# Kernel tuning notes

Hardware: AMD Instinct MI355X
Metric: run time of the kernel (lower is better)

The kernel has to match this reference:

```python
import jax, jax.numpy as jnp
import numpy as np

N, E, H, D, FE = 50000, 400000, 4, 64, 64  # nodes, edges, heads, per-head dim, edge feat dim
NEG_SLOPE = 0.2


def setup_inputs() -> dict:
    key = jax.random.key(0)
    ks = jax.random.split(key, 18)
    def p(k, shape, s=0.1):
        return jax.random.normal(k, shape, dtype=jnp.float32) * s
    return dict(
        features=p(ks[0], (N, D), 1.0),
        edge_feat=p(ks[1], (E, FE), 1.0),
        src=jax.random.randint(ks[2], (E,), 0, N),
        dst=jax.random.randint(ks[3], (E,), 0, N),
        # layer 0: in=64 -> H*D=256, residual Linear since 64 != 256
        W0=p(ks[4], (D, H * D)), We0=p(ks[5], (FE, H * D)),
        al0=p(ks[6], (H, D)), ar0=p(ks[7], (H, D)), ae0=p(ks[8], (H, D)),
        b0=p(ks[9], (H * D,)), Wres0=p(ks[10], (D, H * D)),
        # layer 1 (last): in=256 -> H*D=256, residual = identity view
        W1=p(ks[11], (H * D, H * D)), We1=p(ks[12], (FE, H * D)),
        al1=p(ks[13], (H, D)), ar1=p(ks[14], (H, D)), ae1=p(ks[15], (H, D)),
        b1=p(ks[16], (H * D,)),
    )


def _edge_gat_layer(h, ef, src, dst, W, We, al, ar, ae, b, Wres=None):
    n = h.shape[0]
    ft = (h @ W).reshape(n, H, D)          # (N,H,D) projected node feats
    fe = (ef @ We).reshape(-1, H, D)       # (E,H,D) projected edge feats
    el = jnp.sum(ft * al, axis=-1)         # (N,H)
    er = jnp.sum(ft * ar, axis=-1)         # (N,H)
    ee = jnp.sum(fe * ae, axis=-1)         # (E,H)
    e = el[src] + er[dst] + ee             # (E,H)
    e = jnp.where(e > 0, e, NEG_SLOPE * e)  # leaky_relu(0.2)
    # segment softmax over incoming edges of each dst node
    m = jax.ops.segment_max(jax.lax.stop_gradient(e), dst, num_segments=n)
    ex = jnp.exp(e - m[dst])
    den = jax.ops.segment_sum(ex, dst, num_segments=n)
    a = ex / den[dst]                      # (E,H) attention
    out = jax.ops.segment_sum(ft[src] * a[:, :, None], dst, num_segments=n)  # (N,H,D)
    res = (h @ Wres).reshape(n, H, D) if Wres is not None else h.reshape(n, H, D)
    return out + res + b.reshape(1, H, D)


def reference(features, edge_feat, src, dst,
              W0, We0, al0, ar0, ae0, b0, Wres0,
              W1, We1, al1, ar1, ae1, b1):
    h = _edge_gat_layer(features, edge_feat, src, dst, W0, We0, al0, ar0, ae0, b0, Wres0)
    h = jax.nn.elu(h.reshape(N, H * D))    # flatten heads + ELU between layers
    h = _edge_gat_layer(h, edge_feat, src, dst, W1, We1, al1, ar1, ae1, b1)
    return h.mean(axis=1)                  # (N, D) mean over heads on last layer
```

## Files before the change

kernel.cpp:

```cpp
#include <hip/hip_runtime.h>
#include <hip/hip_bf16.h>

#define NN 50000
#define EE 400000
#define NB 196

typedef __bf16 bf16_8 __attribute__((ext_vector_type(8)));
typedef __bf16 bf16_4 __attribute__((ext_vector_type(4)));
typedef __bf16 bf16_2 __attribute__((ext_vector_type(2)));
typedef float f32x4 __attribute__((ext_vector_type(4)));
typedef float f32x2 __attribute__((ext_vector_type(2)));

__device__ inline f32x2 bf2(unsigned u) {
  f32x2 r;
  r.x = __uint_as_float(u << 16);
  r.y = __uint_as_float(u & 0xffff0000u);
  return r;
}

__global__ __launch_bounds__(256) void prep_kernel(
    const float* __restrict__ features, __bf16* __restrict__ fbf,
    const float* __restrict__ W0, const float* __restrict__ Wres0, __bf16* __restrict__ Bt0,
    const float* __restrict__ W1, __bf16* __restrict__ Bt1,
    const float* __restrict__ We0, const float* __restrict__ ae0, float* __restrict__ Ve0,
    const float* __restrict__ We1, const float* __restrict__ ae1, float* __restrict__ Ve1,
    const int* __restrict__ dst, int* __restrict__ cnt) {
  int b = blockIdx.x;
  int t = threadIdx.x;
  if (b < 1563) {
    int i = b * 256 + t;
    if (i < NN * 64 / 8) {
      const float4* p = (const float4*)features + (size_t)i * 2;
      float4 a = p[0], c = p[1];
      bf16_8 v = {(__bf16)a.x, (__bf16)a.y, (__bf16)a.z, (__bf16)a.w,
                  (__bf16)c.x, (__bf16)c.y, (__bf16)c.z, (__bf16)c.w};
      *(bf16_8*)(fbf + (size_t)i * 8) = v;
    }
  } else if (b < 1563 + 128) {
    int idx = (b - 1563) * 256 + t;
    int j = idx >> 6, k = idx & 63;
    float v = (j < 256) ? W0[k * 256 + j] : Wres0[k * 256 + (j - 256)];
    Bt0[idx] = (__bf16)v;
  } else if (b < 1563 + 128 + 256) {
    int idx = (b - 1563 - 128) * 256 + t;
    int j = idx >> 8, k = idx & 255;
    Bt1[idx] = (__bf16)W1[k * 256 + j];
  } else if (b == 1947) {
    int f = t >> 2, h = t & 3;
    float s = 0.f;
    for (int d = 0; d < 64; ++d) s += We0[f * 256 + h * 64 + d] * ae0[h * 64 + d];
    Ve0[f * 4 + h] = s;
  } else if (b == 1948) {
    int f = t >> 2, h = t & 3;
    float s = 0.f;
    for (int d = 0; d < 64; ++d) s += We1[f * 256 + h * 64 + d] * ae1[h * 64 + d];
    Ve1[f * 4 + h] = s;
  } else {
    int e = (b - 1949) * 256 + t;
    if (e < EE) atomicAdd(&cnt[dst[e]], 1);
  }
}

__global__ __launch_bounds__(256) void scan1_kernel(const int* __restrict__ cnt,
                                                    int* __restrict__ scanbuf,
                                                    int* __restrict__ blocksum) {
  __shared__ int s[256];
  int t = threadIdx.x;
  int idx = blockIdx.x * 256 + t;
  int c = (idx < NN) ? cnt[idx] : 0;
  s[t] = c;
  __syncthreads();
  for (int d = 1; d < 256; d <<= 1) {
    int v = (t >= d) ? s[t - d] : 0;
    __syncthreads();
    s[t] += v;
    __syncthreads();
  }
  if (idx < NN) scanbuf[idx] = s[t];
  if (t == 255) blocksum[blockIdx.x] = s[255];
}

__global__ __launch_bounds__(256) void scan23_kernel(const int* __restrict__ scanbuf,
                                                     const int* __restrict__ cnt,
                                                     const int* __restrict__ blocksum,
                                                     int* __restrict__ off,
                                                     int* __restrict__ cur) {
  __shared__ int s[256];
  int t = threadIdx.x;
  int c = (t < NB) ? blocksum[t] : 0;
  s[t] = c;
  __syncthreads();
  for (int d = 1; d < 256; d <<= 1) {
    int v = (t >= d) ? s[t - d] : 0;
    __syncthreads();
    s[t] += v;
    __syncthreads();
  }
  int boff = (blockIdx.x > 0) ? s[blockIdx.x - 1] : 0;
  int idx = blockIdx.x * 256 + t;
  if (idx < NN) {
    int o = boff + scanbuf[idx] - cnt[idx];
    off[idx] = o;
    cur[idx] = o;
  }
  if (idx == 0) off[NN] = EE;
}

__global__ __launch_bounds__(256) void filleek_kernel(
    const int* __restrict__ src, const int* __restrict__ dst,
    int* __restrict__ cur, int* __restrict__ srcc,
    const float* __restrict__ ef, const float* __restrict__ Ve0,
    const float* __restrict__ Ve1, float* __restrict__ eeoc) {
  int e = blockIdx.x * 256 + threadIdx.x;
  if (e >= EE) return;
  const float4* row = (const float4*)(ef + (size_t)e * 64);
  float4 v[16];
#pragma unroll
  for (int i = 0; i < 16; ++i) v[i] = row[i];
  int d = dst[e], s = src[e];
  int p = atomicAdd(&cur[d], 1);
  srcc[p] = s;
  float a0 = 0, a1 = 0, a2 = 0, a3 = 0;
  float c0 = 0, c1 = 0, c2 = 0, c3 = 0;
#pragma unroll
  for (int i = 0; i < 16; ++i) {
    float xs[4] = {v[i].x, v[i].y, v[i].z, v[i].w};
#pragma unroll
    for (int j = 0; j < 4; ++j) {
      float x = xs[j];
      int f4 = (i * 4 + j) * 4;
      a0 += x * Ve0[f4 + 0]; a1 += x * Ve0[f4 + 1];
      a2 += x * Ve0[f4 + 2]; a3 += x * Ve0[f4 + 3];
      c0 += x * Ve1[f4 + 0]; c1 += x * Ve1[f4 + 1];
      c2 += x * Ve1[f4 + 2]; c3 += x * Ve1[f4 + 3];
    }
  }
  float4 u; u.x = a0; u.y = a1; u.z = a2; u.w = a3;
  float4 w; w.x = c0; w.y = c1; w.z = c2; w.w = c3;
  *(float4*)(eeoc + (size_t)p * 8) = u;
  *(float4*)(eeoc + (size_t)p * 8 + 4) = w;
}

#define LDK 40
__global__ __launch_bounds__(256) void gemm_kernel(const __bf16* __restrict__ A,
                                                   const __bf16* __restrict__ Bt,
                                                   __bf16* __restrict__ ft,
                                                   __bf16* __restrict__ base,
                                                   const float* __restrict__ bias,
                                                   const float* __restrict__ al,
                                                   const float* __restrict__ ar,
                                                   float* __restrict__ el,
                                                   float* __restrict__ er,
                                                   int M, int K) {
  __shared__ __align__(16) __bf16 Al[64 * LDK];
  __shared__ __align__(16) __bf16 Bl[64 * LDK];
  int tid = threadIdx.x;
  int wav = tid >> 6, lane = tid & 63;
  int quad = lane >> 4, l16 = lane & 15;
  int bm = blockIdx.x * 64;
  int bn = blockIdx.y * 64;
  int sr = tid >> 2;
  int sk = (tid & 3) << 3;

  f32x4 acc[4] = {{0, 0, 0, 0}, {0, 0, 0, 0}, {0, 0, 0, 0}, {0, 0, 0, 0}};

  for (int k0 = 0; k0 < K; k0 += 32) {
    uint4 av = {0, 0, 0, 0};
    int arow = bm + sr;
    if (arow < M) av = *(const uint4*)(A + (size_t)arow * K + k0 + sk);
    uint4 bv = *(const uint4*)(Bt + (size_t)(bn + sr) * K + k0 + sk);
    __syncthreads();
    *(uint4*)&Al[sr * LDK + sk] = av;
    *(uint4*)&Bl[sr * LDK + sk] = bv;
    __syncthreads();
    bf16_8 af = *(const bf16_8*)&Al[(wav * 16 + l16) * LDK + quad * 8];
#pragma unroll
    for (int nt = 0; nt < 4; ++nt) {
      bf16_8 bf = *(const bf16_8*)&Bl[(nt * 16 + l16) * LDK + quad * 8];
      acc[nt] = __builtin_amdgcn_mfma_f32_16x16x32_bf16(af, bf, acc[nt], 0, 0, 0);
    }
  }

  int row0 = bm + wav * 16 + quad * 4;

  if (bn < 256) {
    int hb = bn >> 6;
#pragma unroll
    for (int r = 0; r < 4; ++r) {
      float pl = 0.f, pr = 0.f;
#pragma unroll
      for (int nt = 0; nt < 4; ++nt) {
        float v = acc[nt][r];
        int d = nt * 16 + l16;
        pl += v * al[hb * 64 + d];
        pr += v * ar[hb * 64 + d];
      }
#pragma unroll
      for (int o2 = 8; o2 > 0; o2 >>= 1) {
        pl += __shfl_xor(pl, o2);
        pr += __shfl_xor(pr, o2);
      }
      int row = row0 + r;
      if (l16 == 0 && row < M) {
        el[row * 4 + hb] = pl;
        er[row * 4 + hb] = pr;
      }
    }
  }

#pragma unroll
  for (int nt = 0; nt < 4; ++nt) {
    int col = bn + nt * 16 + l16;
#pragma unroll
    for (int r = 0; r < 4; ++r) {
      int row = row0 + r;
      if (row < M) {
        float v = acc[nt][r];
        if (col < 256)
          ft[(size_t)row * 256 + col] = (__bf16)v;
        else
          base[(size_t)row * 256 + (col - 256)] = (__bf16)(v + bias[col - 256]);
      }
    }
  }
}

template <int LAYER>
__global__ __launch_bounds__(256) void agg_kernel(const int* __restrict__ off,
                                                  const int* __restrict__ srcc,
                                                  const float* __restrict__ eeoc,
                                                  const float* __restrict__ el,
                                                  const float* __restrict__ er,
                                                  const __bf16* __restrict__ ft,
                                                  const __bf16* prev,
                                                  const float* __restrict__ bias,
                                                  __bf16* outb,
                                                  float* __restrict__ outf) {
  __shared__ f32x2 wl2[4][16][5];
  int t = threadIdx.x;
  int wav = t >> 6, lane = t & 63;
  int es = lane & 15;
  int head = lane >> 4;
  int n = blockIdx.x * 4 + wav;
  int beg = off[n], end = off[n + 1];
  float ern = er[n * 4 + head];
  int offb = lane * 8;

  const char* ftb = (const char*)ft;
  f32x2 acc0 = {0.f, 0.f}, acc1 = {0.f, 0.f};
  float denp = 0.f;

  for (int c = beg; c < end; c += 16) {
    int rem = end - c;
    if (rem > 16) rem = 16;
    int sv = 0;
    float wv = 0.f;
    if (es < rem) {
      sv = srcc[c + es];
      float z = el[sv * 4 + head] + ern + eeoc[(size_t)(c + es) * 8 + LAYER * 4 + head];
      wv = __expf(z > 0.f ? z : 0.2f * z);
    }
    denp += wv;
    wl2[wav][es][head] = (f32x2){wv, wv};
    int kk = 0;
    for (; kk + 8 <= rem; kk += 8) {
      int s0 = __builtin_amdgcn_readlane(sv, kk);
      int s1 = __builtin_amdgcn_readlane(sv, kk + 1);
      int s2 = __builtin_amdgcn_readlane(sv, kk + 2);
      int s3 = __builtin_amdgcn_readlane(sv, kk + 3);
      int s4 = __builtin_amdgcn_readlane(sv, kk + 4);
      int s5 = __builtin_amdgcn_readlane(sv, kk + 5);
      int s6 = __builtin_amdgcn_readlane(sv, kk + 6);
      int s7 = __builtin_amdgcn_readlane(sv, kk + 7);
      uint2 u0 = *(const uint2*)(ftb + (size_t)s0 * 512 + offb);
      uint2 u1 = *(const uint2*)(ftb + (size_t)s1 * 512 + offb);
      uint2 u2 = *(const uint2*)(ftb + (size_t)s2 * 512 + offb);
      uint2 u3 = *(const uint2*)(ftb + (size_t)s3 * 512 + offb);
      uint2 u4 = *(const uint2*)(ftb + (size_t)s4 * 512 + offb);
      uint2 u5 = *(const uint2*)(ftb + (size_t)s5 * 512 + offb);
      uint2 u6 = *(const uint2*)(ftb + (size_t)s6 * 512 + offb);
      uint2 u7 = *(const uint2*)(ftb + (size_t)s7 * 512 + offb);
      f32x2 w0 = wl2[wav][kk][head];
      f32x2 w1 = wl2[wav][kk + 1][head];
      f32x2 w2 = wl2[wav][kk + 2][head];
      f32x2 w3 = wl2[wav][kk + 3][head];
      f32x2 w4 = wl2[wav][kk + 4][head];
      f32x2 w5 = wl2[wav][kk + 5][head];
      f32x2 w6 = wl2[wav][kk + 6][head];
      f32x2 w7 = wl2[wav][kk + 7][head];
      acc0 = __builtin_elementwise_fma(bf2(u0.x), w0, acc0);
      acc1 = __builtin_elementwise_fma(bf2(u0.y), w0, acc1);
      acc0 = __builtin_elementwise_fma(bf2(u1.x), w1, acc0);
      acc1 = __builtin_elementwise_fma(bf2(u1.y), w1, acc1);
      acc0 = __builtin_elementwise_fma(bf2(u2.x), w2, acc0);
      acc1 = __builtin_elementwise_fma(bf2(u2.y), w2, acc1);
      acc0 = __builtin_elementwise_fma(bf2(u3.x), w3, acc0);
      acc1 = __builtin_elementwise_fma(bf2(u3.y), w3, acc1);
      acc0 = __builtin_elementwise_fma(bf2(u4.x), w4, acc0);
      acc1 = __builtin_elementwise_fma(bf2(u4.y), w4, acc1);
      acc0 = __builtin_elementwise_fma(bf2(u5.x), w5, acc0);
      acc1 = __builtin_elementwise_fma(bf2(u5.y), w5, acc1);
      acc0 = __builtin_elementwise_fma(bf2(u6.x), w6, acc0);
      acc1 = __builtin_elementwise_fma(bf2(u6.y), w6, acc1);
      acc0 = __builtin_elementwise_fma(bf2(u7.x), w7, acc0);
      acc1 = __builtin_elementwise_fma(bf2(u7.y), w7, acc1);
    }
    for (; kk + 4 <= rem; kk += 4) {
      int s0 = __builtin_amdgcn_readlane(sv, kk);
      int s1 = __builtin_amdgcn_readlane(sv, kk + 1);
      int s2 = __builtin_amdgcn_readlane(sv, kk + 2);
      int s3 = __builtin_amdgcn_readlane(sv, kk + 3);
      uint2 u0 = *(const uint2*)(ftb + (size_t)s0 * 512 + offb);
      uint2 u1 = *(const uint2*)(ftb + (size_t)s1 * 512 + offb);
      uint2 u2 = *(const uint2*)(ftb + (size_t)s2 * 512 + offb);
      uint2 u3 = *(const uint2*)(ftb + (size_t)s3 * 512 + offb);
      f32x2 w0 = wl2[wav][kk][head];
      f32x2 w1 = wl2[wav][kk + 1][head];
      f32x2 w2 = wl2[wav][kk + 2][head];
      f32x2 w3 = wl2[wav][kk + 3][head];
      acc0 = __builtin_elementwise_fma(bf2(u0.x), w0, acc0);
      acc1 = __builtin_elementwise_fma(bf2(u0.y), w0, acc1);
      acc0 = __builtin_elementwise_fma(bf2(u1.x), w1, acc0);
      acc1 = __builtin_elementwise_fma(bf2(u1.y), w1, acc1);
      acc0 = __builtin_elementwise_fma(bf2(u2.x), w2, acc0);
      acc1 = __builtin_elementwise_fma(bf2(u2.y), w2, acc1);
      acc0 = __builtin_elementwise_fma(bf2(u3.x), w3, acc0);
      acc1 = __builtin_elementwise_fma(bf2(u3.y), w3, acc1);
    }
    for (; kk < rem; ++kk) {
      int s0 = __builtin_amdgcn_readlane(sv, kk);
      uint2 u0 = *(const uint2*)(ftb + (size_t)s0 * 512 + offb);
      f32x2 w0 = wl2[wav][kk][head];
      acc0 = __builtin_elementwise_fma(bf2(u0.x), w0, acc0);
      acc1 = __builtin_elementwise_fma(bf2(u0.y), w0, acc1);
    }
  }
#pragma unroll
  for (int m = 1; m < 16; m <<= 1) denp += __shfl_xor(denp, m);

  float r0 = 0.f, r1 = 0.f, r2 = 0.f, r3 = 0.f;
  if (end > beg) {
    float rd = 1.f / denp;
    r0 = acc0.x * rd; r1 = acc0.y * rd;
    r2 = acc1.x * rd; r3 = acc1.y * rd;
  }

  uint2 pu = *(const uint2*)((const char*)prev + (size_t)n * 512 + offb);
  f32x2 p0 = bf2(pu.x), p1 = bf2(pu.y);

  if (LAYER == 0) {
    float v0 = r0 + p0.x, v1 = r1 + p0.y;
    float v2 = r2 + p1.x, v3 = r3 + p1.y;
    v0 = v0 > 0.f ? v0 : (__expf(v0) - 1.0f);
    v1 = v1 > 0.f ? v1 : (__expf(v1) - 1.0f);
    v2 = v2 > 0.f ? v2 : (__expf(v2) - 1.0f);
    v3 = v3 > 0.f ? v3 : (__expf(v3) - 1.0f);
    bf16_4 o = {(__bf16)v0, (__bf16)v1, (__bf16)v2, (__bf16)v3};
    *(bf16_4*)((char*)outb + (size_t)n * 512 + offb) = o;
  } else {
    float4 bv = *(const float4*)(bias + lane * 4);
    float s0 = r0 + p0.x + bv.x;
    float s1 = r1 + p0.y + bv.y;
    float s2 = r2 + p1.x + bv.z;
    float s3 = r3 + p1.y + bv.w;
    s0 += __shfl_xor(s0, 16); s0 += __shfl_xor(s0, 32);
    s1 += __shfl_xor(s1, 16); s1 += __shfl_xor(s1, 32);
    s2 += __shfl_xor(s2, 16); s2 += __shfl_xor(s2, 32);
    s3 += __shfl_xor(s3, 16); s3 += __shfl_xor(s3, 32);
    if (head == 0) {
      float4 s;
      s.x = 0.25f * s0; s.y = 0.25f * s1; s.z = 0.25f * s2; s.w = 0.25f * s3;
      *(float4*)(outf + (size_t)n * 64 + es * 4) = s;
    }
  }
}

extern "C" void kernel_launch(void* const* d_in, const int* in_sizes, int n_in,
                              void* d_out, int out_size, void* d_ws, size_t ws_size,
                              hipStream_t stream) {
  const float* features  = (const float*)d_in[0];
  const float* edge_feat = (const float*)d_in[1];
  const int*   src       = (const int*)d_in[2];
  const int*   dst       = (const int*)d_in[3];
  const float* W0    = (const float*)d_in[4];
  const float* We0   = (const float*)d_in[5];
  const float* al0   = (const float*)d_in[6];
  const float* ar0   = (const float*)d_in[7];
  const float* ae0   = (const float*)d_in[8];
  const float* b0    = (const float*)d_in[9];
  const float* Wres0 = (const float*)d_in[10];
  const float* W1    = (const float*)d_in[11];
  const float* We1   = (const float*)d_in[12];
  const float* al1   = (const float*)d_in[13];
  const float* ar1   = (const float*)d_in[14];
  const float* ae1   = (const float*)d_in[15];
  const float* b1    = (const float*)d_in[16];
  float* out = (float*)d_out;

  char* ws = (char*)d_ws;
  size_t o = 0;
  auto alloc = [&](size_t bytes) {
    void* p = ws + o;
    o = (o + bytes + 255) & ~(size_t)255;
    return p;
  };
  int*    cnt      = (int*)alloc((size_t)NN * 4);
  int*    scanbuf  = (int*)alloc((size_t)NN * 4);
  int*    blocksum = (int*)alloc(256 * 4);
  int*    off      = (int*)alloc((size_t)(NN + 1) * 4);
  int*    cur      = (int*)alloc((size_t)NN * 4);
  int*    srcc     = (int*)alloc((size_t)EE * 4);
  float*  eeoc     = (float*)alloc((size_t)EE * 8 * 4);
  float*  el       = (float*)alloc((size_t)NN * 4 * 4);
  float*  er       = (float*)alloc((size_t)NN * 4 * 4);
  float*  Ve0      = (float*)alloc(256 * 4);
  float*  Ve1      = (float*)alloc(256 * 4);
  __bf16* Bt0      = (__bf16*)alloc((size_t)512 * 64 * 2);
  __bf16* Bt1      = (__bf16*)alloc((size_t)256 * 256 * 2);
  __bf16* fbf      = (__bf16*)alloc((size_t)NN * 64 * 2);
  __bf16* ft       = (__bf16*)alloc((size_t)NN * 256 * 2);
  __bf16* base     = (__bf16*)alloc((size_t)NN * 256 * 2);
  __bf16* h1       = base;

  const int EB = (EE + 255) / 256;
  const int MG = (NN + 63) / 64;

  hipMemsetAsync(cnt, 0, (size_t)NN * 4, stream);
  prep_kernel<<<1949 + EB, 256, 0, stream>>>(features, fbf, W0, Wres0, Bt0, W1, Bt1,
                                             We0, ae0, Ve0, We1, ae1, Ve1, dst, cnt);
  scan1_kernel<<<NB, 256, 0, stream>>>(cnt, scanbuf, blocksum);
  scan23_kernel<<<NB, 256, 0, stream>>>(scanbuf, cnt, blocksum, off, cur);
  filleek_kernel<<<EB, 256, 0, stream>>>(src, dst, cur, srcc, edge_feat,
                                         Ve0, Ve1, eeoc);

  gemm_kernel<<<dim3(MG, 8), 256, 0, stream>>>(fbf, Bt0, ft, base, b0, al0, ar0, el, er, NN, 64);
  agg_kernel<0><<<NN / 4, 256, 0, stream>>>(off, srcc, eeoc, el, er, ft, base, nullptr, h1, nullptr);

  gemm_kernel<<<dim3(MG, 4), 256, 0, stream>>>(h1, Bt1, ft, nullptr, nullptr, al1, ar1, el, er, NN, 256);
  agg_kernel<1><<<NN / 4, 256, 0, stream>>>(off, srcc, eeoc, el, er, ft, h1, b1, nullptr, out);
}
```

Measured before the change: 371.9 us.

## Split edge-score kernel across lanes with DPP reduction and edge-ordered scores

The edge feature projection kernel now uses 16 lanes per edge, so each edge row is read with coalesced float4 loads instead of one thread streaming a whole 256-byte row. Partial sums are combined with DPP row-shift adds. Edge scores are stored in original edge order in separate per-layer arrays, and the CSR holds (src, edge id) pairs. This removes the scattered eeoc writes, but the aggregation kernels now do an indirect gather of edge scores and read an 8-byte CSR entry per edge.

```diff
diff --git a/kernel.cpp b/kernel.cpp
--- a/kernel.cpp
+++ b/kernel.cpp
@@ -7,7 +7,6 @@
 
 typedef __bf16 bf16_8 __attribute__((ext_vector_type(8)));
 typedef __bf16 bf16_4 __attribute__((ext_vector_type(4)));
-typedef __bf16 bf16_2 __attribute__((ext_vector_type(2)));
 typedef float f32x4 __attribute__((ext_vector_type(4)));
 typedef float f32x2 __attribute__((ext_vector_type(2)));
 
@@ -15,6 +14,22 @@
   f32x2 r;
   r.x = __uint_as_float(u << 16);
   r.y = __uint_as_float(u & 0xffff0000u);
+  return r;
+}
+
+__device__ inline f32x4 fma4s(float x, f32x4 b, f32x4 a) {
+  f32x4 xs = {x, x, x, x};
+  return __builtin_elementwise_fma(xs, b, a);
+}
+
+template <int CTRL>
+__device__ inline f32x4 dpp_shr_add4(f32x4 a) {
+  f32x4 r;
+#pragma unroll
+  for (int i = 0; i < 4; ++i) {
+    int y = __builtin_amdgcn_mov_dpp(__float_as_int(a[i]), CTRL, 0xF, 0xF, true);
+    r[i] = a[i] + __int_as_float(y);
+  }
   return r;
 }
 
@@ -106,39 +121,51 @@
   if (idx == 0) off[NN] = EE;
 }
 
-__global__ __launch_bounds__(256) void filleek_kernel(
+__global__ __launch_bounds__(256) void eekfill_kernel(
     const int* __restrict__ src, const int* __restrict__ dst,
-    int* __restrict__ cur, int* __restrict__ srcc,
+    int* __restrict__ cur, int2* __restrict__ se_csr,
     const float* __restrict__ ef, const float* __restrict__ Ve0,
-    const float* __restrict__ Ve1, float* __restrict__ eeoc) {
-  int e = blockIdx.x * 256 + threadIdx.x;
-  if (e >= EE) return;
-  const float4* row = (const float4*)(ef + (size_t)e * 64);
-  float4 v[16];
-#pragma unroll
-  for (int i = 0; i < 16; ++i) v[i] = row[i];
-  int d = dst[e], s = src[e];
-  int p = atomicAdd(&cur[d], 1);
-  srcc[p] = s;
-  float a0 = 0, a1 = 0, a2 = 0, a3 = 0;
-  float c0 = 0, c1 = 0, c2 = 0, c3 = 0;
-#pragma unroll
-  for (int i = 0; i < 16; ++i) {
-    float xs[4] = {v[i].x, v[i].y, v[i].z, v[i].w};
-#pragma unroll
-    for (int j = 0; j < 4; ++j) {
-      float x = xs[j];
-      int f4 = (i * 4 + j) * 4;
-      a0 += x * Ve0[f4 + 0]; a1 += x * Ve0[f4 + 1];
-      a2 += x * Ve0[f4 + 2]; a3 += x * Ve0[f4 + 3];
-      c0 += x * Ve1[f4 + 0]; c1 += x * Ve1[f4 + 1];
-      c2 += x * Ve1[f4 + 2]; c3 += x * Ve1[f4 + 3];
-    }
-  }
-  float4 u; u.x = a0; u.y = a1; u.z = a2; u.w = a3;
-  float4 w; w.x = c0; w.y = c1; w.z = c2; w.w = c3;
-  *(float4*)(eeoc + (size_t)p * 8) = u;
-  *(float4*)(eeoc + (size_t)p * 8 + 4) = w;
+    const float* __restrict__ Ve1, float* __restrict__ ee0,
+    float* __restrict__ ee1) {
+  int t = threadIdx.x;
+  int wav = t >> 6, lane = t & 63;
+  int fg = lane & 15;
+  int eg = lane >> 4;
+  int e = blockIdx.x * 16 + wav * 4 + eg;
+
+  f32x4 x4 = *(const f32x4*)(ef + (size_t)e * 64 + fg * 4);
+
+  f32x4 v0[4], v1[4];
+#pragma unroll
+  for (int j = 0; j < 4; ++j) {
+    v0[j] = *(const f32x4*)(Ve0 + (fg * 4 + j) * 4);
+    v1[j] = *(const f32x4*)(Ve1 + (fg * 4 + j) * 4);
+  }
+
+  int s = 0, p = 0;
+  if (fg == 15) {
+    s = src[e];
+    int d = dst[e];
+    p = atomicAdd(&cur[d], 1);
+  }
+
+  f32x4 a0 = {0, 0, 0, 0}, a1 = {0, 0, 0, 0};
+#pragma unroll
+  for (int j = 0; j < 4; ++j) {
+    float x = x4[j];
+    a0 = fma4s(x, v0[j], a0);
+    a1 = fma4s(x, v1[j], a1);
+  }
+  a0 = dpp_shr_add4<0x111>(a0); a1 = dpp_shr_add4<0x111>(a1);
+  a0 = dpp_shr_add4<0x112>(a0); a1 = dpp_shr_add4<0x112>(a1);
+  a0 = dpp_shr_add4<0x114>(a0); a1 = dpp_shr_add4<0x114>(a1);
+  a0 = dpp_shr_add4<0x118>(a0); a1 = dpp_shr_add4<0x118>(a1);
+
+  if (fg == 15) {
+    *(f32x4*)(ee0 + (size_t)e * 4) = a0;
+    *(f32x4*)(ee1 + (size_t)e * 4) = a1;
+    se_csr[p] = make_int2(s, e);
+  }
 }
 
 #define LDK 40
@@ -227,8 +254,8 @@
 
 template <int LAYER>
 __global__ __launch_bounds__(256) void agg_kernel(const int* __restrict__ off,
-                                                  const int* __restrict__ srcc,
-                                                  const float* __restrict__ eeoc,
+                                                  const int2* __restrict__ se_csr,
+                                                  const float* __restrict__ eeL,
                                                   const float* __restrict__ el,
                                                   const float* __restrict__ er,
                                                   const __bf16* __restrict__ ft,
@@ -256,8 +283,9 @@
     int sv = 0;
     float wv = 0.f;
     if (es < rem) {
-      sv = srcc[c + es];
-      float z = el[sv * 4 + head] + ern + eeoc[(size_t)(c + es) * 8 + LAYER * 4 + head];
+      int2 se = se_csr[c + es];
+      sv = se.x;
+      float z = el[sv * 4 + head] + ern + eeL[(size_t)se.y * 4 + head];
       wv = __expf(z > 0.f ? z : 0.2f * z);
     }
     denp += wv;
@@ -409,8 +437,9 @@
   int*    blocksum = (int*)alloc(256 * 4);
   int*    off      = (int*)alloc((size_t)(NN + 1) * 4);
   int*    cur      = (int*)alloc((size_t)NN * 4);
-  int*    srcc     = (int*)alloc((size_t)EE * 4);
-  float*  eeoc     = (float*)alloc((size_t)EE * 8 * 4);
+  int2*   se_csr   = (int2*)alloc((size_t)EE * 8);
+  float*  ee0      = (float*)alloc((size_t)EE * 4 * 4);
+  float*  ee1      = (float*)alloc((size_t)EE * 4 * 4);
   float*  el       = (float*)alloc((size_t)NN * 4 * 4);
   float*  er       = (float*)alloc((size_t)NN * 4 * 4);
   float*  Ve0      = (float*)alloc(256 * 4);
@@ -430,12 +459,12 @@
                                              We0, ae0, Ve0, We1, ae1, Ve1, dst, cnt);
   scan1_kernel<<<NB, 256, 0, stream>>>(cnt, scanbuf, blocksum);
   scan23_kernel<<<NB, 256, 0, stream>>>(scanbuf, cnt, blocksum, off, cur);
-  filleek_kernel<<<EB, 256, 0, stream>>>(src, dst, cur, srcc, edge_feat,
-                                         Ve0, Ve1, eeoc);
+  eekfill_kernel<<<EE / 16, 256, 0, stream>>>(src, dst, cur, se_csr, edge_feat,
+                                              Ve0, Ve1, ee0, ee1);
 
   gemm_kernel<<<dim3(MG, 8), 256, 0, stream>>>(fbf, Bt0, ft, base, b0, al0, ar0, el, er, NN, 64);
-  agg_kernel<0><<<NN / 4, 256, 0, stream>>>(off, srcc, eeoc, el, er, ft, base, nullptr, h1, nullptr);
+  agg_kernel<0><<<NN / 4, 256, 0, stream>>>(off, se_csr, ee0, el, er, ft, base, nullptr, h1, nullptr);
 
   gemm_kernel<<<dim3(MG, 4), 256, 0, stream>>>(h1, Bt1, ft, nullptr, nullptr, al1, ar1, el, er, NN, 256);
-  agg_kernel<1><<<NN / 4, 256, 0, stream>>>(off, srcc, eeoc, el, er, ft, h1, b1, nullptr, out);
-}
+  agg_kernel<1><<<NN / 4, 256, 0, stream>>>(off, se_csr, ee1, el, er, ft, h1, b1, nullptr, out);
+}
```

Measured after the change: 389.1 us. 4.6% more time.
